# Performance work log

Measured on AMD Instinct MI355X. Metric: run time of the kernel, lower is better.

The kernel has to match this reference:

```python
import math
import jax, jax.numpy as jnp
import numpy as np

NTYPE, C, H, E = 3, 256, 8, 32  # n_embd=256, n_head=8, edge_dim=32
A1 = 16  # aux_x1 feature dim (aux_x2 dim = E - A1)


def setup_inputs() -> dict:
    key = jax.random.key(0)
    ks = jax.random.split(key, 16)
    B, T1, T2 = 8, 128, 256
    s = 0.02
    return {
        "x1": jax.random.normal(ks[0], (B, T1, C), jnp.float32),
        "x2": jax.random.normal(ks[1], (B, T2, C), jnp.float32),
        "aux_x1": jax.random.normal(ks[2], (B, T1, A1), jnp.float32),
        "aux_x2": jax.random.normal(ks[3], (B, T2, E - A1), jnp.float32),
        "masks": jax.random.randint(ks[4], (NTYPE, B, T1, T2), 0, 2, jnp.int32),
        # per-type linear params, stored (in, out) so y = x @ W + b
        "Wq": jax.random.normal(ks[5], (NTYPE, C, C), jnp.float32) * s,
        "bq": jnp.zeros((NTYPE, C), jnp.float32),
        "Wk": jax.random.normal(ks[6], (NTYPE, C + E, C), jnp.float32) * s,
        "bk": jnp.zeros((NTYPE, C), jnp.float32),
        "Wv": jax.random.normal(ks[7], (NTYPE, C + E, C), jnp.float32) * s,
        "bv": jnp.zeros((NTYPE, C), jnp.float32),
        "Wp": jax.random.normal(ks[8], (NTYPE, C, C), jnp.float32) * s,
        "bp": jnp.zeros((NTYPE, C), jnp.float32),
    }


def _aux_attn(x1, x2, aux_x1, aux_x2, mask, Wq, bq, Wk, bk, Wv, bv, Wp, bp):
    """One AuxCrossAttention type. mask: (B,T1,T2) int."""
    B, T1, _ = x1.shape
    T2 = x2.shape[1]
    hd = C // H
    scale = 1.0 / math.sqrt(hd)

    q = x1 @ Wq + bq  # (B,T1,C)
    # k/v over aug_x2 = [x2 | aux_x1 | aux_x2]; split the linear instead of
    # materializing the (B,T1,T2,C+E) concat (same math by linearity).
    Wk_x, Wk_a1, Wk_a2 = Wk[:C], Wk[C:C + A1], Wk[C + A1:]
    Wv_x, Wv_a1, Wv_a2 = Wv[:C], Wv[C:C + A1], Wv[C + A1:]
    k = (x2 @ Wk_x + aux_x2 @ Wk_a2 + bk)[:, None] + (aux_x1 @ Wk_a1)[:, :, None]  # (B,T1,T2,C)
    v = (x2 @ Wv_x + aux_x2 @ Wv_a2 + bv)[:, None] + (aux_x1 @ Wv_a1)[:, :, None]  # (B,T1,T2,C)

    qh = q.reshape(B, T1, H, hd)
    kh = k.reshape(B, T1, T2, H, hd)
    vh = v.reshape(B, T1, T2, H, hd)

    att = jnp.einsum("bthd,btshd->bhts", qh, kh) * scale  # (B,H,T1,T2)
    valid = (mask != 0)[:, None]  # (B,1,T1,T2)
    att = jnp.where(valid, att, -jnp.inf)
    all_masked = (mask == 0).all(-1)  # (B,T1)
    att = jnp.where(all_masked[:, None, :, None], 0.0, att)
    f = jnp.finfo(att.dtype)
    att = jnp.nan_to_num(att, nan=0.0, posinf=f.max, neginf=f.min)
    att = jax.nn.softmax(att, axis=-1)

    y = jnp.einsum("bhts,btshd->bthd", att, vh).reshape(B, T1, C)
    return y @ Wp + bp


def reference(x1, x2, aux_x1, aux_x2, masks, Wq, bq, Wk, bk, Wv, bv, Wp, bp):
    resid = jnp.zeros_like(x1)
    for i in range(NTYPE):
        resid = resid + _aux_attn(x1, x2, aux_x1, aux_x2, masks[i],
                                  Wq[i], bq[i], Wk[i], bk[i], Wv[i], bv[i], Wp[i], bp[i])
    return resid
```

## Files before the change

### kernel.cpp

```cpp
#include <hip/hip_runtime.h>
#include <hip/hip_bf16.h>

#define NC 256
#define HD 32

typedef __attribute__((ext_vector_type(8))) short short8;
typedef __attribute__((ext_vector_type(4))) short short4v;
typedef __attribute__((ext_vector_type(4))) float f32x4;

#define QSC (0.17677669529663687f * 1.4426950408889634f)

__device__ __forceinline__ unsigned short f2bf(float f) {
    union { float f; unsigned u; } v; v.f = f;
    unsigned r = v.u + 0x7fffu + ((v.u >> 16) & 1u);
    return (unsigned short)(r >> 16);
}
__device__ __forceinline__ short8 cvt8(float4 a, float4 b) {
    short8 s;
    s[0] = (short)f2bf(a.x); s[1] = (short)f2bf(a.y);
    s[2] = (short)f2bf(a.z); s[3] = (short)f2bf(a.w);
    s[4] = (short)f2bf(b.x); s[5] = (short)f2bf(b.y);
    s[6] = (short)f2bf(b.z); s[7] = (short)f2bf(b.w);
    return s;
}

__global__ __launch_bounds__(256) void prep(
    const float* __restrict__ x1, const float* __restrict__ x2,
    const float* __restrict__ ax1, const float* __restrict__ ax2,
    const int* __restrict__ masks,
    const float* __restrict__ Wq, const float* __restrict__ Wk,
    const float* __restrict__ Wv, const float* __restrict__ Wp,
    short* __restrict__ x1b, short* __restrict__ A2, short* __restrict__ ax1p,
    unsigned int* __restrict__ mb,
    short* __restrict__ WqT, short* __restrict__ WkT, short* __restrict__ WvT,
    short* __restrict__ WpT)
{
    const int bx = blockIdx.x, tid = threadIdx.x;
    const short8 zero8 = {0, 0, 0, 0, 0, 0, 0, 0};

    if (bx < 64) {
        const size_t base = ((size_t)bx * 256 + tid) * 16;
        const float* p = x1 + base;
        float4 a = *(const float4*)p,       b = *(const float4*)(p + 4);
        float4 c = *(const float4*)(p + 8), d = *(const float4*)(p + 12);
        *(short8*)&x1b[base]     = cvt8(a, b);
        *(short8*)&x1b[base + 8] = cvt8(c, d);
    } else if (bx < 352) {
        const int g = (bx - 64) * 256 + tid;
        const int row = g / 36, c8 = g - row * 36;
        short8 s;
        if (c8 < 32) {
            const float* p = x2 + (size_t)row * 256 + c8 * 8;
            s = cvt8(*(const float4*)p, *(const float4*)(p + 4));
        } else if (c8 < 34) {
            const float* p = ax2 + (size_t)row * 16 + (c8 - 32) * 8;
            s = cvt8(*(const float4*)p, *(const float4*)(p + 4));
        } else {
            s = zero8;
        }
        *(short8*)&A2[(size_t)row * 288 + c8 * 8] = s;
    } else if (bx < 356) {
        const int row = (bx - 352) * 256 + tid;
        const float* p = ax1 + (size_t)row * 16;
        float4 a = *(const float4*)p,       b = *(const float4*)(p + 4);
        float4 c = *(const float4*)(p + 8), d = *(const float4*)(p + 12);
        short* o = ax1p + (size_t)row * 32;
        *(short8*)o        = cvt8(a, b);
        *(short8*)(o + 8)  = cvt8(c, d);
        *(short8*)(o + 16) = zero8;
        *(short8*)(o + 24) = zero8;
    } else if (bx < 548) {
        const int r0 = (bx - 356) * 16;
        const int wave = tid >> 6, lane = tid & 63;
        for (int rr = 0; rr < 16; ++rr) {
            const int row = r0 + rr;
            const int mk = masks[(size_t)row * 256 + tid];
            unsigned long long bal = __ballot(mk != 0);
            if (lane == 0) {
                mb[row * 8 + wave * 2 + 0] = (unsigned int)bal;
                mb[row * 8 + wave * 2 + 1] = (unsigned int)(bal >> 32);
            }
        }
    } else if (bx < 644) {
        const int idx = bx - 548, i = idx >> 5, k8 = idx & 31;
        const int n = tid;
        const float* W = Wq + (size_t)i * 256 * 256;
        short8 s;
#pragma unroll
        for (int j = 0; j < 8; ++j) s[j] = (short)f2bf(W[(size_t)(k8 * 8 + j) * 256 + n]);
        *(short8*)&WqT[(size_t)i * 256 * 256 + (size_t)n * 256 + k8 * 8] = s;
    } else if (bx < 860) {
        const int idx0 = bx - 644;
        const int kv = idx0 / 108, idx = idx0 % 108;
        const int i = idx / 36, k8 = idx % 36;
        const int n = tid;
        const float* W = (kv ? Wv : Wk) + (size_t)i * 288 * 256;
        short* O = (kv ? WvT : WkT) + (size_t)i * 256 * 288;
        short8 s;
#pragma unroll
        for (int j = 0; j < 8; ++j) {
            const int kp = k8 * 8 + j;
            const int src = (kp < 256) ? kp : (kp < 272 ? kp + 16 : -1);
            s[j] = (src >= 0) ? (short)f2bf(W[(size_t)src * 256 + n]) : (short)0;
        }
        *(short8*)&O[(size_t)n * 288 + k8 * 8] = s;
    } else {
        const int idx = bx - 860, i = idx >> 5, k8 = idx & 31;
        const int n = tid;
        const float* W = Wp + (size_t)i * 256 * 256;
        short8 s;
#pragma unroll
        for (int j = 0; j < 8; ++j) s[j] = (short)f2bf(W[(size_t)(k8 * 8 + j) * 256 + n]);
        *(short8*)&WpT[(size_t)i * 256 * 256 + (size_t)n * 256 + k8 * 8] = s;
    }
}

__global__ __launch_bounds__(256) void qkv_attn(
    const short* __restrict__ x1b, const short* __restrict__ A2,
    const short* __restrict__ WqT, const short* __restrict__ WkT,
    const short* __restrict__ WvT, const float* __restrict__ Wv,
    const short* __restrict__ WpT,
    const float* __restrict__ bq, const float* __restrict__ bk,
    const float* __restrict__ bv, const unsigned int* __restrict__ mb,
    short* __restrict__ yb, short* __restrict__ WeffT)
{
    const int tid = threadIdx.x;
    const int wave = tid >> 6, lane = tid & 63;
    const int qd = lane >> 4, ml = lane & 15;
    const int bx = blockIdx.x;

    if (bx == 384) {
        f32x4 wacc[4];
#pragma unroll
        for (int nt = 0; nt < 4; ++nt) wacc[nt] = {0.f, 0.f, 0.f, 0.f};
        for (int i = 0; i < 3; ++i) {
            const float* Wvp = Wv + (size_t)i * 288 * 256;
            const short* Wpt = WpT + (size_t)i * 256 * 256;
            for (int step = 0; step < 8; ++step) {
                const float* ap = Wvp + (size_t)(256 + ml) * 256 + step * 32 + qd * 8;
                short8 af = cvt8(*(const float4*)ap, *(const float4*)(ap + 4));
#pragma unroll
                for (int nt = 0; nt < 4; ++nt) {
                    const int n = (wave * 4 + nt) * 16 + ml;
                    short8 bf = *(const short8*)&Wpt[(size_t)n * 256 + step * 32 + qd * 8];
                    wacc[nt] = __builtin_amdgcn_mfma_f32_16x16x32_bf16(af, bf, wacc[nt], 0, 0, 0);
                }
            }
        }
#pragma unroll
        for (int nt = 0; nt < 4; ++nt) {
            const int n = (wave * 4 + nt) * 16 + ml;
#pragma unroll
            for (int r = 0; r < 4; ++r) {
                WeffT[n * 32 + qd * 4 + r] = (short)f2bf(wacc[nt][r]);
                WeffT[n * 32 + 16 + qd * 4 + r] = 0;
            }
        }
        return;
    }

    const int b = bx & 7;
    const int rest = bx >> 3;
    const int i = rest >> 4;
    const int h = (rest >> 1) & 7;
    const int tc = rest & 1;
    const size_t bb = (size_t)i * 8 + b;
    const int hc = h * 32;

    __shared__ short q_s[64][40];
    __shared__ short k_s[256][40];
    __shared__ short vT_s[32][264];
    __shared__ short P_s[4][2048];

    const short* Wq_i = WqT + (size_t)i * 256 * 256;
    const short* Wk_i = WkT + (size_t)i * 256 * 288;
    const short* Wv_i = WvT + (size_t)i * 256 * 288;

    f32x4 qacc[2], kacc[4][2], vacc[4][2];
#pragma unroll
    for (int nt = 0; nt < 2; ++nt) qacc[nt] = {0.f, 0.f, 0.f, 0.f};
#pragma unroll
    for (int mt = 0; mt < 4; ++mt)
#pragma unroll
        for (int nt = 0; nt < 2; ++nt) {
            kacc[mt][nt] = {0.f, 0.f, 0.f, 0.f};
            vacc[mt][nt] = {0.f, 0.f, 0.f, 0.f};
        }

    for (int step = 0; step < 8; ++step) {
        short8 afq, bfq[2], af[4], bfk[2], bfv[2];
        afq = *(const short8*)&x1b[(size_t)(b * 128 + tc * 64 + wave * 16 + ml) * 256 + step * 32 + qd * 8];
#pragma unroll
        for (int nt = 0; nt < 2; ++nt)
            bfq[nt] = *(const short8*)&Wq_i[(size_t)(hc + nt * 16 + ml) * 256 + step * 32 + qd * 8];
#pragma unroll
        for (int mt = 0; mt < 4; ++mt)
            af[mt] = *(const short8*)&A2[(size_t)(b * 256 + wave * 64 + mt * 16 + ml) * 288 + step * 32 + qd * 8];
#pragma unroll
        for (int nt = 0; nt < 2; ++nt) {
            bfk[nt] = *(const short8*)&Wk_i[(size_t)(hc + nt * 16 + ml) * 288 + step * 32 + qd * 8];
            bfv[nt] = *(const short8*)&Wv_i[(size_t)(hc + nt * 16 + ml) * 288 + step * 32 + qd * 8];
        }
#pragma unroll
        for (int nt = 0; nt < 2; ++nt)
            qacc[nt] = __builtin_amdgcn_mfma_f32_16x16x32_bf16(afq, bfq[nt], qacc[nt], 0, 0, 0);
#pragma unroll
        for (int mt = 0; mt < 4; ++mt)
#pragma unroll
            for (int nt = 0; nt < 2; ++nt) {
                kacc[mt][nt] = __builtin_amdgcn_mfma_f32_16x16x32_bf16(af[mt], bfk[nt], kacc[mt][nt], 0, 0, 0);
                vacc[mt][nt] = __builtin_amdgcn_mfma_f32_16x16x32_bf16(af[mt], bfv[nt], vacc[mt][nt], 0, 0, 0);
            }
    }
    {
        const int step = 8;
        short8 af[4], bfk[2], bfv[2];
#pragma unroll
        for (int mt = 0; mt < 4; ++mt)
            af[mt] = *(const short8*)&A2[(size_t)(b * 256 + wave * 64 + mt * 16 + ml) * 288 + step * 32 + qd * 8];
#pragma unroll
        for (int nt = 0; nt < 2; ++nt) {
            bfk[nt] = *(const short8*)&Wk_i[(size_t)(hc + nt * 16 + ml) * 288 + step * 32 + qd * 8];
            bfv[nt] = *(const short8*)&Wv_i[(size_t)(hc + nt * 16 + ml) * 288 + step * 32 + qd * 8];
        }
#pragma unroll
        for (int mt = 0; mt < 4; ++mt)
#pragma unroll
            for (int nt = 0; nt < 2; ++nt) {
                kacc[mt][nt] = __builtin_amdgcn_mfma_f32_16x16x32_bf16(af[mt], bfk[nt], kacc[mt][nt], 0, 0, 0);
                vacc[mt][nt] = __builtin_amdgcn_mfma_f32_16x16x32_bf16(af[mt], bfv[nt], vacc[mt][nt], 0, 0, 0);
            }
    }

#pragma unroll
    for (int nt = 0; nt < 2; ++nt) {
        const float bsq = bq[i * 256 + hc + nt * 16 + ml];
        const int r0 = wave * 16 + qd * 4;
#pragma unroll
        for (int r = 0; r < 4; ++r)
            q_s[r0 + r][nt * 16 + ml] = (short)f2bf((qacc[nt][r] + bsq) * QSC);
    }
#pragma unroll
    for (int nt = 0; nt < 2; ++nt) {
        const float bsk = bk[i * 256 + hc + nt * 16 + ml];
        const float bsvv = bv[i * 256 + hc + nt * 16 + ml];
#pragma unroll
        for (int mt = 0; mt < 4; ++mt) {
            const int s0 = wave * 64 + mt * 16 + qd * 4;
#pragma unroll
            for (int r = 0; r < 4; ++r)
                k_s[s0 + r][nt * 16 + ml] = (short)f2bf(kacc[mt][nt][r] + bsk);
            short4v s;
            s.x = (short)f2bf(vacc[mt][nt][0] + bsvv);
            s.y = (short)f2bf(vacc[mt][nt][1] + bsvv);
            s.z = (short)f2bf(vacc[mt][nt][2] + bsvv);
            s.w = (short)f2bf(vacc[mt][nt][3] + bsvv);
            *(short4v*)&vT_s[nt * 16 + ml][s0] = s;
        }
    }
    __syncthreads();

    short* Pw = &P_s[wave][0];
    {
        const int tloc = wave * 16;
        const int tb = tc * 64 + tloc + qd * 4;

        uint4 wlo[4], whi[4];
#pragma unroll
        for (int r = 0; r < 4; ++r) {
            const unsigned int* p = mb + (bb * 128 + tb + r) * 8;
            wlo[r] = *(const uint4*)p;
            whi[r] = *(const uint4*)(p + 4);
        }

        short8 af = *(const short8*)&q_s[tloc + ml][qd * 8];

        f32x4 sacc[16];
#pragma unroll
        for (int nt = 0; nt < 16; ++nt) sacc[nt] = {0.f, 0.f, 0.f, 0.f};
#pragma unroll
        for (int nt = 0; nt < 16; ++nt) {
            short8 bf = *(const short8*)&k_s[nt * 16 + ml][qd * 8];
            sacc[nt] = __builtin_amdgcn_mfma_f32_16x16x32_bf16(af, bf, sacc[nt], 0, 0, 0);
        }

        f32x4 rs = {0.f, 0.f, 0.f, 0.f};
#pragma unroll
        for (int nt = 0; nt < 16; ++nt) {
#pragma unroll
            for (int r = 0; r < 4; ++r) {
                unsigned int w;
                switch (nt >> 1) {
                    case 0: w = wlo[r].x; break; case 1: w = wlo[r].y; break;
                    case 2: w = wlo[r].z; break; case 3: w = wlo[r].w; break;
                    case 4: w = whi[r].x; break; case 5: w = whi[r].y; break;
                    case 6: w = whi[r].z; break; default: w = whi[r].w; break;
                }
                const bool mk = (w >> ((nt & 1) * 16 + ml)) & 1u;
                float e = mk ? __builtin_amdgcn_exp2f(sacc[nt][r]) : 0.f;
                sacc[nt][r] = e;
                rs[r] += e;
            }
        }
#pragma unroll
        for (int off = 1; off <= 8; off <<= 1) {
#pragma unroll
            for (int r = 0; r < 4; ++r) rs[r] += __shfl_xor(rs[r], off);
        }
        f32x4 pinv, pfill;
#pragma unroll
        for (int r = 0; r < 4; ++r) {
            const bool z = (rs[r] == 0.f);
            pinv[r]  = z ? 0.f : 1.f / rs[r];
            pfill[r] = z ? (1.f / 256.f) : 0.f;
        }

        f32x4 oacc[2];
        oacc[0] = {0.f, 0.f, 0.f, 0.f};
        oacc[1] = {0.f, 0.f, 0.f, 0.f};
#pragma unroll
        for (int half = 0; half < 2; ++half) {
#pragma unroll
            for (int nt8 = 0; nt8 < 8; ++nt8) {
                const int nt = half * 8 + nt8;
                const int sgrp = 2 * nt8 + (ml >> 3);
                const int pos = ml & 7;
#pragma unroll
                for (int r = 0; r < 4; ++r) {
                    const float p = sacc[nt][r] * pinv[r] + pfill[r];
                    Pw[(sgrp * 16 + qd * 4 + r) * 8 + pos] = (short)f2bf(p);
                }
            }
#pragma unroll
            for (int ksl = 0; ksl < 4; ++ksl) {
                const int ks = half * 4 + ksl;
                short8 pa = *(const short8*)&Pw[((ksl * 4 + qd) * 16 + ml) * 8];
#pragma unroll
                for (int n2 = 0; n2 < 2; ++n2) {
                    short8 vf = *(const short8*)&vT_s[n2 * 16 + ml][ks * 32 + qd * 8];
                    oacc[n2] = __builtin_amdgcn_mfma_f32_16x16x32_bf16(pa, vf, oacc[n2], 0, 0, 0);
                }
            }
        }

#pragma unroll
        for (int n2 = 0; n2 < 2; ++n2) {
            const int d = hc + n2 * 16 + ml;
#pragma unroll
            for (int r = 0; r < 4; ++r)
                yb[(size_t)(bb * 128 + tb + r) * 256 + d] = (short)f2bf(oacc[n2][r]);
        }
    }
}

__global__ __launch_bounds__(256) void proj2(
    const short* __restrict__ yb, const short* __restrict__ WpT,
    const short* __restrict__ ax1p, const short* __restrict__ WeffT,
    const float* __restrict__ bp, float* __restrict__ out)
{
    const int bx = blockIdx.x;
    const int m0 = (bx >> 2) * 16, n0 = (bx & 3) * 64;
    const int tid = threadIdx.x;
    const int wave = tid >> 6, lane = tid & 63;
    const int qd = lane >> 4, ml = lane & 15;
    const int col = n0 + wave * 16 + ml;

    f32x4 acc = {0.f, 0.f, 0.f, 0.f};

    for (int i = 0; i < 3; ++i) {
        const short* A = yb + (size_t)i * 1024 * 256;
        const short* W = WpT + (size_t)i * 256 * 256;
#pragma unroll
        for (int step = 0; step < 8; ++step) {
            short8 af = *(const short8*)&A[(size_t)(m0 + ml) * 256 + step * 32 + qd * 8];
            short8 bf = *(const short8*)&W[(size_t)col * 256 + step * 32 + qd * 8];
            acc = __builtin_amdgcn_mfma_f32_16x16x32_bf16(af, bf, acc, 0, 0, 0);
        }
    }
    {
        short8 af = *(const short8*)&ax1p[(size_t)(m0 + ml) * 32 + qd * 8];
        short8 bf = *(const short8*)&WeffT[(size_t)col * 32 + qd * 8];
        acc = __builtin_amdgcn_mfma_f32_16x16x32_bf16(af, bf, acc, 0, 0, 0);
    }
    const float b3 = bp[col] + bp[256 + col] + bp[512 + col];
    const int row0 = m0 + qd * 4;
#pragma unroll
    for (int r = 0; r < 4; ++r)
        out[(size_t)(row0 + r) * 256 + col] = acc[r] + b3;
}

extern "C" void kernel_launch(void* const* d_in, const int* in_sizes, int n_in,
                              void* d_out, int out_size, void* d_ws, size_t ws_size,
                              hipStream_t stream)
{
    const float* x1  = (const float*)d_in[0];
    const float* x2  = (const float*)d_in[1];
    const float* ax1 = (const float*)d_in[2];
    const float* ax2 = (const float*)d_in[3];
    const int*   mk  = (const int*)d_in[4];
    const float* Wq  = (const float*)d_in[5];
    const float* bq  = (const float*)d_in[6];
    const float* Wk  = (const float*)d_in[7];
    const float* bk  = (const float*)d_in[8];
    const float* Wv  = (const float*)d_in[9];
    const float* bv  = (const float*)d_in[10];
    const float* Wp  = (const float*)d_in[11];
    const float* bp  = (const float*)d_in[12];

    char* w = (char*)d_ws;
    short* x1b   = (short*)(w + 0);
    short* A2    = (short*)(w + 524288);
    short* ax1p  = (short*)(w + 1703936);
    short* WqT   = (short*)(w + 1769472);
    short* WkT   = (short*)(w + 2162688);
    short* WvT   = (short*)(w + 2605056);
    short* WpT   = (short*)(w + 3047424);
    unsigned int* mbits = (unsigned int*)(w + 3440640);
    short* WeffT = (short*)(w + 3538944);
    short* yb    = (short*)(w + 3555328);

    prep<<<dim3(956), 256, 0, stream>>>(x1, x2, ax1, ax2, mk, Wq, Wk, Wv, Wp,
                                        x1b, A2, ax1p, mbits, WqT, WkT, WvT, WpT);
    qkv_attn<<<dim3(385), 256, 0, stream>>>(x1b, A2, WqT, WkT, WvT, Wv, WpT,
                                            bq, bk, bv, mbits, yb, WeffT);
    proj2<<<dim3(256), 256, 0, stream>>>(yb, WpT, ax1p, WeffT, bp, (float*)d_out);
}
```

Baseline: 120.1 us.

## Merge query-tile blocks into 1024-thread blocks to stop recomputing K/V projections

Each (type, batch, head) now runs as one 1024-thread block covering all 128 query rows, where before two blocks split the queries and each recomputed the full K/V projection for that head. The K/V projection is spread across 16 waves, one 16-row tile each, and only the first 8 waves compute Q and run the attention phase. The P staging buffer is shrunk and the P·V loop is reworked into quarters to fit the larger q_s. The aim is to halve the redundant K/V GEMM work. In exchange there are half as many blocks, 8 waves sit idle during attention, and 1024-thread blocks may lower occupancy.

```diff
diff --git a/kernel.cpp b/kernel.cpp
--- a/kernel.cpp
+++ b/kernel.cpp
@@ -115,7 +115,7 @@
     }
 }
 
-__global__ __launch_bounds__(256) void qkv_attn(
+__global__ __launch_bounds__(1024) void qkv_attn(
     const short* __restrict__ x1b, const short* __restrict__ A2,
     const short* __restrict__ WqT, const short* __restrict__ WkT,
     const short* __restrict__ WvT, const float* __restrict__ Wv,
@@ -129,7 +129,8 @@
     const int qd = lane >> 4, ml = lane & 15;
     const int bx = blockIdx.x;
 
-    if (bx == 384) {
+    if (bx == 192) {
+        if (wave >= 4) return;
         f32x4 wacc[4];
 #pragma unroll
         for (int nt = 0; nt < 4; ++nt) wacc[nt] = {0.f, 0.f, 0.f, 0.f};
@@ -159,111 +160,100 @@
         return;
     }
 
-    const int b = bx & 7;
-    const int rest = bx >> 3;
-    const int i = rest >> 4;
-    const int h = (rest >> 1) & 7;
-    const int tc = rest & 1;
+    const int i = bx >> 6, b = (bx >> 3) & 7, h = bx & 7;
     const size_t bb = (size_t)i * 8 + b;
     const int hc = h * 32;
 
-    __shared__ short q_s[64][40];
+    __shared__ short q_s[128][40];
     __shared__ short k_s[256][40];
     __shared__ short vT_s[32][264];
-    __shared__ short P_s[4][2048];
+    __shared__ short P_s[8][1024];
 
     const short* Wq_i = WqT + (size_t)i * 256 * 256;
     const short* Wk_i = WkT + (size_t)i * 256 * 288;
     const short* Wv_i = WvT + (size_t)i * 256 * 288;
 
-    f32x4 qacc[2], kacc[4][2], vacc[4][2];
-#pragma unroll
-    for (int nt = 0; nt < 2; ++nt) qacc[nt] = {0.f, 0.f, 0.f, 0.f};
-#pragma unroll
-    for (int mt = 0; mt < 4; ++mt)
-#pragma unroll
-        for (int nt = 0; nt < 2; ++nt) {
-            kacc[mt][nt] = {0.f, 0.f, 0.f, 0.f};
-            vacc[mt][nt] = {0.f, 0.f, 0.f, 0.f};
-        }
+    f32x4 qacc[2], kacc[2], vacc[2];
+#pragma unroll
+    for (int nt = 0; nt < 2; ++nt) {
+        qacc[nt] = {0.f, 0.f, 0.f, 0.f};
+        kacc[nt] = {0.f, 0.f, 0.f, 0.f};
+        vacc[nt] = {0.f, 0.f, 0.f, 0.f};
+    }
 
     for (int step = 0; step < 8; ++step) {
-        short8 afq, bfq[2], af[4], bfk[2], bfv[2];
-        afq = *(const short8*)&x1b[(size_t)(b * 128 + tc * 64 + wave * 16 + ml) * 256 + step * 32 + qd * 8];
-#pragma unroll
-        for (int nt = 0; nt < 2; ++nt)
-            bfq[nt] = *(const short8*)&Wq_i[(size_t)(hc + nt * 16 + ml) * 256 + step * 32 + qd * 8];
-#pragma unroll
-        for (int mt = 0; mt < 4; ++mt)
-            af[mt] = *(const short8*)&A2[(size_t)(b * 256 + wave * 64 + mt * 16 + ml) * 288 + step * 32 + qd * 8];
+        short8 afq, bfq[2], af, bfk[2], bfv[2];
+        if (wave < 8) {
+            afq = *(const short8*)&x1b[(size_t)(b * 128 + wave * 16 + ml) * 256 + step * 32 + qd * 8];
+#pragma unroll
+            for (int nt = 0; nt < 2; ++nt)
+                bfq[nt] = *(const short8*)&Wq_i[(size_t)(hc + nt * 16 + ml) * 256 + step * 32 + qd * 8];
+        }
+        af = *(const short8*)&A2[(size_t)(b * 256 + wave * 16 + ml) * 288 + step * 32 + qd * 8];
 #pragma unroll
         for (int nt = 0; nt < 2; ++nt) {
             bfk[nt] = *(const short8*)&Wk_i[(size_t)(hc + nt * 16 + ml) * 288 + step * 32 + qd * 8];
             bfv[nt] = *(const short8*)&Wv_i[(size_t)(hc + nt * 16 + ml) * 288 + step * 32 + qd * 8];
         }
-#pragma unroll
-        for (int nt = 0; nt < 2; ++nt)
-            qacc[nt] = __builtin_amdgcn_mfma_f32_16x16x32_bf16(afq, bfq[nt], qacc[nt], 0, 0, 0);
-#pragma unroll
-        for (int mt = 0; mt < 4; ++mt)
-#pragma unroll
-            for (int nt = 0; nt < 2; ++nt) {
-                kacc[mt][nt] = __builtin_amdgcn_mfma_f32_16x16x32_bf16(af[mt], bfk[nt], kacc[mt][nt], 0, 0, 0);
-                vacc[mt][nt] = __builtin_amdgcn_mfma_f32_16x16x32_bf16(af[mt], bfv[nt], vacc[mt][nt], 0, 0, 0);
-            }
+        if (wave < 8) {
+#pragma unroll
+            for (int nt = 0; nt < 2; ++nt)
+                qacc[nt] = __builtin_amdgcn_mfma_f32_16x16x32_bf16(afq, bfq[nt], qacc[nt], 0, 0, 0);
+        }
+#pragma unroll
+        for (int nt = 0; nt < 2; ++nt) {
+            kacc[nt] = __builtin_amdgcn_mfma_f32_16x16x32_bf16(af, bfk[nt], kacc[nt], 0, 0, 0);
+            vacc[nt] = __builtin_amdgcn_mfma_f32_16x16x32_bf16(af, bfv[nt], vacc[nt], 0, 0, 0);
+        }
     }
     {
         const int step = 8;
-        short8 af[4], bfk[2], bfv[2];
-#pragma unroll
-        for (int mt = 0; mt < 4; ++mt)
-            af[mt] = *(const short8*)&A2[(size_t)(b * 256 + wave * 64 + mt * 16 + ml) * 288 + step * 32 + qd * 8];
+        short8 af, bfk[2], bfv[2];
+        af = *(const short8*)&A2[(size_t)(b * 256 + wave * 16 + ml) * 288 + step * 32 + qd * 8];
 #pragma unroll
         for (int nt = 0; nt < 2; ++nt) {
             bfk[nt] = *(const short8*)&Wk_i[(size_t)(hc + nt * 16 + ml) * 288 + step * 32 + qd * 8];
             bfv[nt] = *(const short8*)&Wv_i[(size_t)(hc + nt * 16 + ml) * 288 + step * 32 + qd * 8];
         }
 #pragma unroll
-        for (int mt = 0; mt < 4; ++mt)
-#pragma unroll
-            for (int nt = 0; nt < 2; ++nt) {
-                kacc[mt][nt] = __builtin_amdgcn_mfma_f32_16x16x32_bf16(af[mt], bfk[nt], kacc[mt][nt], 0, 0, 0);
-                vacc[mt][nt] = __builtin_amdgcn_mfma_f32_16x16x32_bf16(af[mt], bfv[nt], vacc[mt][nt], 0, 0, 0);
-            }
-    }
-
-#pragma unroll
-    for (int nt = 0; nt < 2; ++nt) {
-        const float bsq = bq[i * 256 + hc + nt * 16 + ml];
-        const int r0 = wave * 16 + qd * 4;
-#pragma unroll
-        for (int r = 0; r < 4; ++r)
-            q_s[r0 + r][nt * 16 + ml] = (short)f2bf((qacc[nt][r] + bsq) * QSC);
+        for (int nt = 0; nt < 2; ++nt) {
+            kacc[nt] = __builtin_amdgcn_mfma_f32_16x16x32_bf16(af, bfk[nt], kacc[nt], 0, 0, 0);
+            vacc[nt] = __builtin_amdgcn_mfma_f32_16x16x32_bf16(af, bfv[nt], vacc[nt], 0, 0, 0);
+        }
+    }
+
+    if (wave < 8) {
+#pragma unroll
+        for (int nt = 0; nt < 2; ++nt) {
+            const float bsq = bq[i * 256 + hc + nt * 16 + ml];
+            const int r0 = wave * 16 + qd * 4;
+#pragma unroll
+            for (int r = 0; r < 4; ++r)
+                q_s[r0 + r][nt * 16 + ml] = (short)f2bf((qacc[nt][r] + bsq) * QSC);
+        }
     }
 #pragma unroll
     for (int nt = 0; nt < 2; ++nt) {
         const float bsk = bk[i * 256 + hc + nt * 16 + ml];
         const float bsvv = bv[i * 256 + hc + nt * 16 + ml];
-#pragma unroll
-        for (int mt = 0; mt < 4; ++mt) {
-            const int s0 = wave * 64 + mt * 16 + qd * 4;
-#pragma unroll
-            for (int r = 0; r < 4; ++r)
-                k_s[s0 + r][nt * 16 + ml] = (short)f2bf(kacc[mt][nt][r] + bsk);
-            short4v s;
-            s.x = (short)f2bf(vacc[mt][nt][0] + bsvv);
-            s.y = (short)f2bf(vacc[mt][nt][1] + bsvv);
-            s.z = (short)f2bf(vacc[mt][nt][2] + bsvv);
-            s.w = (short)f2bf(vacc[mt][nt][3] + bsvv);
-            *(short4v*)&vT_s[nt * 16 + ml][s0] = s;
-        }
+        const int s0 = wave * 16 + qd * 4;
+#pragma unroll
+        for (int r = 0; r < 4; ++r)
+            k_s[s0 + r][nt * 16 + ml] = (short)f2bf(kacc[nt][r] + bsk);
+        short4v s;
+        s.x = (short)f2bf(vacc[nt][0] + bsvv);
+        s.y = (short)f2bf(vacc[nt][1] + bsvv);
+        s.z = (short)f2bf(vacc[nt][2] + bsvv);
+        s.w = (short)f2bf(vacc[nt][3] + bsvv);
+        *(short4v*)&vT_s[nt * 16 + ml][s0] = s;
     }
     __syncthreads();
 
+    if (wave >= 8) return;
     short* Pw = &P_s[wave][0];
     {
-        const int tloc = wave * 16;
-        const int tb = tc * 64 + tloc + qd * 4;
+        const int t0 = wave * 16;
+        const int tb = t0 + qd * 4;
 
         uint4 wlo[4], whi[4];
 #pragma unroll
@@ -273,7 +263,7 @@
             whi[r] = *(const uint4*)(p + 4);
         }
 
-        short8 af = *(const short8*)&q_s[tloc + ml][qd * 8];
+        short8 af = *(const short8*)&q_s[t0 + ml][qd * 8];
 
         f32x4 sacc[16];
 #pragma unroll
@@ -319,11 +309,11 @@
         oacc[0] = {0.f, 0.f, 0.f, 0.f};
         oacc[1] = {0.f, 0.f, 0.f, 0.f};
 #pragma unroll
-        for (int half = 0; half < 2; ++half) {
-#pragma unroll
-            for (int nt8 = 0; nt8 < 8; ++nt8) {
-                const int nt = half * 8 + nt8;
-                const int sgrp = 2 * nt8 + (ml >> 3);
+        for (int quar = 0; quar < 4; ++quar) {
+#pragma unroll
+            for (int nt4 = 0; nt4 < 4; ++nt4) {
+                const int nt = quar * 4 + nt4;
+                const int sgrp = 2 * nt4 + (ml >> 3);
                 const int pos = ml & 7;
 #pragma unroll
                 for (int r = 0; r < 4; ++r) {
@@ -332,8 +322,8 @@
                 }
             }
 #pragma unroll
-            for (int ksl = 0; ksl < 4; ++ksl) {
-                const int ks = half * 4 + ksl;
+            for (int ksl = 0; ksl < 2; ++ksl) {
+                const int ks = quar * 2 + ksl;
                 short8 pa = *(const short8*)&Pw[((ksl * 4 + qd) * 16 + ml) * 8];
 #pragma unroll
                 for (int n2 = 0; n2 < 2; ++n2) {
@@ -421,7 +411,7 @@
 
     prep<<<dim3(956), 256, 0, stream>>>(x1, x2, ax1, ax2, mk, Wq, Wk, Wv, Wp,
                                         x1b, A2, ax1p, mbits, WqT, WkT, WvT, WpT);
-    qkv_attn<<<dim3(385), 256, 0, stream>>>(x1b, A2, WqT, WkT, WvT, Wv, WpT,
-                                            bq, bk, bv, mbits, yb, WeffT);
+    qkv_attn<<<dim3(193), 1024, 0, stream>>>(x1b, A2, WqT, WkT, WvT, Wv, WpT,
+                                             bq, bk, bv, mbits, yb, WeffT);
     proj2<<<dim3(256), 256, 0, stream>>>(yb, WpT, ax1p, WeffT, bp, (float*)d_out);
 }
```

Result: faster. 116.2 us (-3.2%).
